# Kernel tuning notes

Measured on AMD Instinct MI355X. Metric: run time of the kernel, lower is better.

Reference implementation:

```python
import jax, jax.numpy as jnp
import numpy as np

COEF_MEMORY = 0.2

def setup_inputs() -> dict:
    key = jax.random.key(0)
    k1, k2, k3, k4 = jax.random.split(key, 4)
    B, T, HW, C, Cv, M = 2, 8, 4096, 64, 3, 1024
    k = jax.random.normal(k1, (B, T, HW, C), dtype=jnp.float32)
    v = jax.random.normal(k2, (B, T, HW, Cv), dtype=jnp.float32)
    m_k = jax.random.normal(k3, (B, T - 1, M, C), dtype=jnp.float32)
    m_v = jax.random.normal(k4, (B, T - 1, M, Cv), dtype=jnp.float32)
    return {"k": k, "v": v, "m_k": m_k, "m_v": m_v}

def reference(k, v, m_k, m_v):
    # k: [B,T,HW,C] frame keys; v: [B,T,HW,Cv] frame values (quarter-res images)
    # m_k: [B,T-1,M,C] memory keys at step i; m_v: [B,T-1,M,Cv] memory values
    c = COEF_MEMORY
    k_i = k[:, :-1]  # ref keys  [B,T-1,HW,C]
    k_j = k[:, 1:]   # tar keys  [B,T-1,HW,C]
    v_i = v[:, :-1]  # ref vals  [B,T-1,HW,Cv]
    # frame-to-frame affinity: softmax over ref positions (last axis)
    sim_k = jax.nn.softmax(jnp.einsum('btqc,btkc->btqk', k_j, k_i), axis=-1)
    # memory-to-frame affinity: softmax over memory slots
    sim_m = jax.nn.softmax(jnp.einsum('btqc,btmc->btqm', k_j, m_k), axis=-1)
    rec_k = jnp.einsum('btqk,btkd->btqd', sim_k, v_i)   # [B,T-1,HW,Cv]
    rec_m = jnp.einsum('btqm,btmd->btqd', sim_m, m_v)   # [B,T-1,HW,Cv]
    return (1.0 - c) * rec_k + c * rec_m
```

## Files before the change

### kernel.cpp

```cpp
#include <hip/hip_runtime.h>

typedef __attribute__((ext_vector_type(2))) __fp16 h2;
typedef __attribute__((ext_vector_type(4))) __fp16 h4;
typedef __attribute__((ext_vector_type(8))) __fp16 h8;
typedef __attribute__((ext_vector_type(4))) float f32x4;

#define LOG2E 1.44269504088896340736f

#define WS_K    0ull
#define WS_MK   7340032ull
#define WS_VT   9175040ull
#define WS_MVT  9633792ull
#define WS_NEED 9748480ull

__device__ __forceinline__ h2 pkrtz(float a, float b) {
    return __builtin_bit_cast(h2, __builtin_amdgcn_cvt_pkrtz(a, b));
}

__device__ __forceinline__ void gll16(const void* g, void* l) {
    __builtin_amdgcn_global_load_lds(
        (const __attribute__((address_space(1))) unsigned int*)g,
        (__attribute__((address_space(3))) unsigned int*)l, 16, 0, 0);
}

__global__ __launch_bounds__(256) void kast_pre_kernel(
    const float* __restrict__ K, const float* __restrict__ V,
    const float* __restrict__ MK, const float* __restrict__ MV,
    char* __restrict__ ws)
{
    const int id = blockIdx.x * 256 + threadIdx.x;
    if (id < 573440) {
        const bool ismk = id >= 458752;
        const int lid = ismk ? id - 458752 : id;
        const int c = lid & 7;
        const int r = (lid >> 3) & 63;
        int kt, s;
        if (ismk) { kt = (lid >> 9) & 15; s = lid >> 13; }
        else      { kt = (lid >> 9) & 63; s = lid >> 15; }
        const int b = s / 7, t = s - b * 7;
        const float* src = ismk
            ? MK + (((size_t)(b * 7 + t) * 1024 + kt * 64 + r) * 64 + c * 8)
            : K  + (((size_t)(b * 8 + t) * 4096 + kt * 64 + r) * 64 + c * 8);
        const f32x4 xa = *(const f32x4*)src;
        const f32x4 xb = *(const f32x4*)(src + 4);
        const h2 q0 = pkrtz(xa[0], xa[1]), q1 = pkrtz(xa[2], xa[3]);
        const h2 q2 = pkrtz(xb[0], xb[1]), q3 = pkrtz(xb[2], xb[3]);
        const h8 out = {q0[0], q0[1], q1[0], q1[1], q2[0], q2[1], q3[0], q3[1]};
        __fp16* dst = (__fp16*)(ws + (ismk ? WS_MK : WS_K))
                    + (size_t)(ismk ? (s * 16 + kt) : (s * 64 + kt)) * 4096
                    + r * 64 + ((c ^ (r & 7)) * 8);
        *(h8*)dst = out;
    } else {
        const int vid = id - 573440;
        const bool ismv = vid >= 57344;
        const int lid = ismv ? vid - 57344 : vid;
        const int c = lid & 15;
        const int d = (lid >> 4) & 3;
        int kt, s;
        if (ismv) { kt = (lid >> 6) & 15; s = lid >> 10; }
        else      { kt = (lid >> 6) & 63; s = lid >> 12; }
        const int b = s / 7, t = s - b * 7;
        const float* src = ismv
            ? MV + (((size_t)(b * 7 + t) * 1024 + kt * 64 + c * 4) * 3)
            : V  + (((size_t)(b * 8 + t) * 4096 + kt * 64 + c * 4) * 3);
        float f0, f1, f2, f3;
        if (d == 3) { f0 = f1 = f2 = f3 = 1.0f; }
        else { f0 = src[d]; f1 = src[3 + d]; f2 = src[6 + d]; f3 = src[9 + d]; }
        const h2 pa = pkrtz(f0, f1), pb = pkrtz(f2, f3);
        const h4 out4 = {pa[0], pa[1], pb[0], pb[1]};
        __fp16* dst = (__fp16*)(ws + (ismv ? WS_MVT : WS_VT))
                    + (size_t)(ismv ? (s * 16 + kt) : (s * 64 + kt)) * 256
                    + d * 64 + (4 * ((c >> 2) ^ d) + (c & 3)) * 4;
        *(h4*)dst = out4;
    }
}

__global__ __launch_bounds__(512) void kast_attn_kernel(
    const float* __restrict__ K,
    const char* __restrict__ ws,
    float* __restrict__ OUT)
{
    __shared__ alignas(16) __fp16 sK2[2][2][64][64];
    __shared__ alignas(16) __fp16 sVT2[2][2][4][64];
    __shared__ float mrg[8][16][10];

    const int id = blockIdx.x;
    const int sw = (id & 7) * 112 + (id >> 3);
    const int bt = sw >> 6;
    const int qblk = sw & 63;
    const int b = bt / 7, t = bt - b * 7;

    const int tid = threadIdx.x;
    const int lane = tid & 63;
    const int w = tid >> 6;
    const int h = w >> 2;
    const int wl = w & 3;
    const int col = lane & 15;
    const int g = lane >> 4;
    const int cs = col & 7;
    const int d3 = col & 3;

    const float* qp = K + (((size_t)b * 8 + (t + 1)) * 4096 + (size_t)(qblk * 64 + wl * 16 + col)) * 64;
    h8 aq[2];
#pragma unroll
    for (int ch = 0; ch < 2; ++ch) {
        const int cc = ch * 32 + g * 8;
        const f32x4 xa = *(const f32x4*)&qp[cc];
        const f32x4 xb = *(const f32x4*)&qp[cc + 4];
        const h2 p0 = pkrtz(xa[0] * LOG2E, xa[1] * LOG2E);
        const h2 p1 = pkrtz(xa[2] * LOG2E, xa[3] * LOG2E);
        const h2 p2 = pkrtz(xb[0] * LOG2E, xb[1] * LOG2E);
        const h2 p3 = pkrtz(xb[2] * LOG2E, xb[3] * LOG2E);
        aq[ch] = (h8){p0[0], p0[1], p1[0], p1[1], p2[0], p2[1], p3[0], p3[1]};
    }

    auto stage = [&](const char* kb, const char* vb, int tkt, int buf) {
        const char* ksrc = kb + (size_t)tkt * 8192 + wl * 2048 + lane * 16;
        char* kdst = ((char*)&sK2[h][buf][0][0]) + wl * 2048 + lane * 16;
        gll16(ksrc, kdst);
        gll16(ksrc + 1024, kdst + 1024);
        if (wl == 0 && lane < 32)
            ((f32x4*)&sVT2[h][buf][0][0])[lane] =
                ((const f32x4*)(vb + (size_t)tkt * 512))[lane];
    };

#pragma unroll
    for (int phase = 0; phase < 2; ++phase) {
        const char* kbase; const char* vbase; int ntile;
        if (phase == 0) {
            ntile = 32;
            kbase = ws + WS_K  + ((size_t)bt * 64 + h * 32) * 8192;
            vbase = ws + WS_VT + ((size_t)bt * 64 + h * 32) * 512;
        } else {
            ntile = 8;
            kbase = ws + WS_MK  + ((size_t)bt * 16 + h * 8) * 8192;
            vbase = ws + WS_MVT + ((size_t)bt * 16 + h * 8) * 512;
        }

        stage(kbase, vbase, 0, 0);
        __syncthreads();

        float mrun = -1e30f;
        f32x4 O = (f32x4){0.f, 0.f, 0.f, 0.f};

        for (int kt = 0; kt < ntile; ++kt) {
            const int cur = kt & 1;
            const int nb = cur ^ 1;

            if (kt + 1 < ntile) stage(kbase, vbase, kt + 1, nb);

            f32x4 acc[4];
#pragma unroll
            for (int nt = 0; nt < 4; ++nt) acc[nt] = (f32x4){0.f, 0.f, 0.f, 0.f};
            __builtin_amdgcn_s_setprio(1);
#pragma unroll
            for (int ch = 0; ch < 2; ++ch) {
                h8 bh[4];
#pragma unroll
                for (int nt = 0; nt < 4; ++nt)
                    bh[nt] = *(const h8*)&sK2[h][cur][nt * 16 + col][((ch * 4 + g) ^ cs) * 8];
#pragma unroll
                for (int nt = 0; nt < 4; ++nt)
                    acc[nt] = __builtin_amdgcn_mfma_f32_16x16x32_f16(bh[nt], aq[ch], acc[nt], 0, 0, 0);
            }
            __builtin_amdgcn_s_setprio(0);

            {
                float tm = acc[0][0];
#pragma unroll
                for (int nt = 0; nt < 4; ++nt)
#pragma unroll
                    for (int j = 0; j < 4; ++j) tm = fmaxf(tm, acc[nt][j]);
                tm = fmaxf(tm, __shfl_xor(tm, 16));
                tm = fmaxf(tm, __shfl_xor(tm, 32));
                if (!__all(tm <= mrun)) {
                    const float mnew = fmaxf(mrun, tm);
                    const float sc = __builtin_amdgcn_exp2f(mrun - mnew);
                    O *= sc;
                    mrun = mnew;
                }
            }

            const char* vtb = (const char*)&sVT2[h][cur][0][0] + d3 * 128;
#pragma unroll
            for (int nt = 0; nt < 4; ++nt) {
                const float p0 = __builtin_amdgcn_exp2f(acc[nt][0] - mrun);
                const float p1 = __builtin_amdgcn_exp2f(acc[nt][1] - mrun);
                const float p2 = __builtin_amdgcn_exp2f(acc[nt][2] - mrun);
                const float p3 = __builtin_amdgcn_exp2f(acc[nt][3] - mrun);
                const h2 pa = pkrtz(p0, p1), pb = pkrtz(p2, p3);
                const h4 pf = (h4){pa[0], pa[1], pb[0], pb[1]};
                const h4 vf = *(const h4*)(vtb + (4 * (nt ^ d3) + g) * 8);
                O = __builtin_amdgcn_mfma_f32_16x16x16f16(vf, pf, O, 0, 0, 0);
            }

            __syncthreads();
        }

        if (g == 0) {
            float* m5 = &mrg[w][col][phase * 5];
            m5[0] = mrun; m5[1] = O[0]; m5[2] = O[1]; m5[3] = O[2]; m5[4] = O[3];
        }
    }

    __syncthreads();
    if (w < 4 && g == 0) {
        const float* A = &mrg[w][col][0];
        const float* B = &mrg[w + 4][col][0];
        float o0 = 0.f, o1 = 0.f, o2 = 0.f;
#pragma unroll
        for (int p = 0; p < 2; ++p) {
            const float wgt = p ? 0.2f : 0.8f;
            const float ma = A[p * 5], mb = B[p * 5];
            const float m = fmaxf(ma, mb);
            const float ea = __builtin_amdgcn_exp2f(ma - m);
            const float eb = __builtin_amdgcn_exp2f(mb - m);
            const float l = A[p * 5 + 4] * ea + B[p * 5 + 4] * eb;
            const float inv = wgt / l;
            o0 += (A[p * 5 + 1] * ea + B[p * 5 + 1] * eb) * inv;
            o1 += (A[p * 5 + 2] * ea + B[p * 5 + 2] * eb) * inv;
            o2 += (A[p * 5 + 3] * ea + B[p * 5 + 3] * eb) * inv;
        }
        const int q = qblk * 64 + w * 16 + col;
        float* op = OUT + (((size_t)b * 7 + t) * 4096 + (size_t)q) * 3;
        op[0] = o0; op[1] = o1; op[2] = o2;
    }
}

__global__ __launch_bounds__(256) void kast_attn_fb(
    const float* __restrict__ K, const float* __restrict__ V,
    const float* __restrict__ MK, const float* __restrict__ MV,
    float* __restrict__ OUT)
{
    __shared__ alignas(16) __fp16 sK[2][64][64];
    __shared__ alignas(16) __fp16 sVT[2][4][68];

    const int id = blockIdx.x;
    const int sw = (id & 7) * 112 + (id >> 3);
    const int bt = sw >> 6;
    const int qblk = sw & 63;
    const int b = bt / 7, t = bt % 7;

    const int tid = threadIdx.x;
    const int lane = tid & 63;
    const int w = tid >> 6;
    const int col = lane & 15;
    const int g = lane >> 4;

    const int r = tid >> 2;
    const int c0 = (tid & 3) * 16;
    const int rs = (r & 7) << 3;
    const unsigned vr = (unsigned)tid / 3u;
    const unsigned vd = (unsigned)tid - vr * 3u;

    if (tid < 128) sVT[tid >> 6][3][tid & 63] = (__fp16)1.0f;

    const float* Qbase = K + (((size_t)b * 8 + (t + 1)) * 4096) * 64;
    h8 aq[2];
    {
        const int qrow = qblk * 64 + w * 16 + col;
        const float* qp = Qbase + (size_t)qrow * 64;
#pragma unroll
        for (int ch = 0; ch < 2; ++ch) {
            const int cc = ch * 32 + g * 8;
            const f32x4 xa = *(const f32x4*)&qp[cc];
            const f32x4 xb = *(const f32x4*)&qp[cc + 4];
            const h2 p0 = pkrtz(xa[0] * LOG2E, xa[1] * LOG2E);
            const h2 p1 = pkrtz(xa[2] * LOG2E, xa[3] * LOG2E);
            const h2 p2 = pkrtz(xb[0] * LOG2E, xb[1] * LOG2E);
            const h2 p3 = pkrtz(xb[2] * LOG2E, xb[3] * LOG2E);
            aq[ch] = (h8){p0[0], p0[1], p1[0], p1[1], p2[0], p2[1], p3[0], p3[1]};
        }
    }

    float outc0 = 0.f, outc1 = 0.f, outc2 = 0.f;

    for (int phase = 0; phase < 2; ++phase) {
        const float* kp; const float* vp; int ntile; float wgt;
        if (phase == 0) {
            kp = K + (((size_t)b * 8 + t) * 4096) * 64;
            vp = V + (((size_t)b * 8 + t) * 4096) * 3;
            ntile = 64; wgt = 0.8f;
        } else {
            kp = MK + (((size_t)b * 7 + t) * 1024) * 64;
            vp = MV + (((size_t)b * 7 + t) * 1024) * 3;
            ntile = 16; wgt = 0.2f;
        }
        {
            const float* src = kp + ((size_t)r) * 64 + c0;
            const f32x4* s4 = (const f32x4*)src;
            const f32x4 ra = s4[0], rb = s4[1], rc = s4[2], rd = s4[3];
            const h2 q0 = pkrtz(ra[0], ra[1]), q1 = pkrtz(ra[2], ra[3]);
            const h2 q2 = pkrtz(rb[0], rb[1]), q3 = pkrtz(rb[2], rb[3]);
            const h2 q4 = pkrtz(rc[0], rc[1]), q5 = pkrtz(rc[2], rc[3]);
            const h2 q6 = pkrtz(rd[0], rd[1]), q7 = pkrtz(rd[2], rd[3]);
            *(h8*)&sK[0][r][c0 ^ rs] = (h8){q0[0], q0[1], q1[0], q1[1], q2[0], q2[1], q3[0], q3[1]};
            *(h8*)&sK[0][r][(c0 + 8) ^ rs] = (h8){q4[0], q4[1], q5[0], q5[1], q6[0], q6[1], q7[0], q7[1]};
            if (tid < 192) sVT[0][vd][vr] = (__fp16)vp[tid];
        }
        __syncthreads();

        float mrun = -1e30f;
        f32x4 O = (f32x4){0.f, 0.f, 0.f, 0.f};

        for (int kt = 0; kt < ntile; ++kt) {
            const int cur = kt & 1;
            const bool have = (kt + 1) < ntile;
            f32x4 ra, rb, rc, rd; float rv = 0.f;
            if (have) {
                const float* src = kp + ((size_t)(kt + 1) * 64 + r) * 64 + c0;
                const f32x4* s4 = (const f32x4*)src;
                ra = s4[0]; rb = s4[1]; rc = s4[2]; rd = s4[3];
                if (tid < 192) rv = vp[(size_t)(kt + 1) * 192 + tid];
            }
            f32x4 acc[4];
#pragma unroll
            for (int nt = 0; nt < 4; ++nt) acc[nt] = (f32x4){0.f, 0.f, 0.f, 0.f};
#pragma unroll
            for (int ch = 0; ch < 2; ++ch) {
                h8 bh[4];
#pragma unroll
                for (int nt = 0; nt < 4; ++nt) {
                    const int rr = nt * 16 + col;
                    const int cc = (ch * 32 + g * 8) ^ ((rr & 7) << 3);
                    bh[nt] = *(const h8*)&sK[cur][rr][cc];
                }
#pragma unroll
                for (int nt = 0; nt < 4; ++nt)
                    acc[nt] = __builtin_amdgcn_mfma_f32_16x16x32_f16(bh[nt], aq[ch], acc[nt], 0, 0, 0);
            }
            {
                float tm = acc[0][0];
#pragma unroll
                for (int nt = 0; nt < 4; ++nt)
#pragma unroll
                    for (int j = 0; j < 4; ++j) tm = fmaxf(tm, acc[nt][j]);
                tm = fmaxf(tm, __shfl_xor(tm, 16));
                tm = fmaxf(tm, __shfl_xor(tm, 32));
                if (!__all(tm <= mrun)) {
                    const float mnew = fmaxf(mrun, tm);
                    const float sc = __builtin_amdgcn_exp2f(mrun - mnew);
                    O *= sc;
                    mrun = mnew;
                }
            }
#pragma unroll
            for (int nt = 0; nt < 4; ++nt) {
                const float p0 = __builtin_amdgcn_exp2f(acc[nt][0] - mrun);
                const float p1 = __builtin_amdgcn_exp2f(acc[nt][1] - mrun);
                const float p2 = __builtin_amdgcn_exp2f(acc[nt][2] - mrun);
                const float p3 = __builtin_amdgcn_exp2f(acc[nt][3] - mrun);
                const h2 pa = pkrtz(p0, p1), pb = pkrtz(p2, p3);
                const h4 pf = (h4){pa[0], pa[1], pb[0], pb[1]};
                const h4 vf = *(const h4*)&sVT[cur][col & 3][nt * 16 + 4 * g];
                O = __builtin_amdgcn_mfma_f32_16x16x16f16(vf, pf, O, 0, 0, 0);
            }
            if (have) {
                const int nb = cur ^ 1;
                const h2 q0 = pkrtz(ra[0], ra[1]), q1 = pkrtz(ra[2], ra[3]);
                const h2 q2 = pkrtz(rb[0], rb[1]), q3 = pkrtz(rb[2], rb[3]);
                const h2 q4 = pkrtz(rc[0], rc[1]), q5 = pkrtz(rc[2], rc[3]);
                const h2 q6 = pkrtz(rd[0], rd[1]), q7 = pkrtz(rd[2], rd[3]);
                *(h8*)&sK[nb][r][c0 ^ rs] = (h8){q0[0], q0[1], q1[0], q1[1], q2[0], q2[1], q3[0], q3[1]};
                *(h8*)&sK[nb][r][(c0 + 8) ^ rs] = (h8){q4[0], q4[1], q5[0], q5[1], q6[0], q6[1], q7[0], q7[1]};
                if (tid < 192) sVT[nb][vd][vr] = (__fp16)rv;
            }
            __syncthreads();
        }
        const float inv = wgt / O[3];
        outc0 += O[0] * inv;
        outc1 += O[1] * inv;
        outc2 += O[2] * inv;
    }

    if (g == 0) {
        const int q = qblk * 64 + w * 16 + col;
        float* op = OUT + (((size_t)b * 7 + t) * 4096 + (size_t)q) * 3;
        op[0] = outc0; op[1] = outc1; op[2] = outc2;
    }
}

extern "C" void kernel_launch(void* const* d_in, const int* in_sizes, int n_in,
                              void* d_out, int out_size, void* d_ws, size_t ws_size,
                              hipStream_t stream) {
    const float* K  = (const float*)d_in[0];
    const float* V  = (const float*)d_in[1];
    const float* MK = (const float*)d_in[2];
    const float* MV = (const float*)d_in[3];
    float* OUT = (float*)d_out;
    if (ws_size >= WS_NEED) {
        hipLaunchKernelGGL(kast_pre_kernel, dim3(2520), dim3(256), 0, stream,
                           K, V, MK, MV, (char*)d_ws);
        hipLaunchKernelGGL(kast_attn_kernel, dim3(896), dim3(512), 0, stream,
                           K, (const char*)d_ws, OUT);
    } else {
        hipLaunchKernelGGL(kast_attn_fb, dim3(896), dim3(256), 0, stream,
                           K, V, MK, MV, OUT);
    }
}
```

Before: 96.87 us.

## Retile waves to 2x2 query-key MFMA tiles with four-way softmax merge

Measured after the change: 118.1 us. +21.9%, slower.

```diff
diff --git a/kernel.cpp b/kernel.cpp
--- a/kernel.cpp
+++ b/kernel.cpp
@@ -82,7 +82,7 @@
 {
     __shared__ alignas(16) __fp16 sK2[2][2][64][64];
     __shared__ alignas(16) __fp16 sVT2[2][2][4][64];
-    __shared__ float mrg[8][16][10];
+    __shared__ float mrg[8][32][5];
 
     const int id = blockIdx.x;
     const int sw = (id & 7) * 112 + (id >> 3);
@@ -95,23 +95,29 @@
     const int w = tid >> 6;
     const int h = w >> 2;
     const int wl = w & 3;
+    const int qsub = wl >> 1;
+    const int ntp = wl & 1;
     const int col = lane & 15;
     const int g = lane >> 4;
     const int cs = col & 7;
     const int d3 = col & 3;
 
-    const float* qp = K + (((size_t)b * 8 + (t + 1)) * 4096 + (size_t)(qblk * 64 + wl * 16 + col)) * 64;
-    h8 aq[2];
-#pragma unroll
-    for (int ch = 0; ch < 2; ++ch) {
-        const int cc = ch * 32 + g * 8;
-        const f32x4 xa = *(const f32x4*)&qp[cc];
-        const f32x4 xb = *(const f32x4*)&qp[cc + 4];
-        const h2 p0 = pkrtz(xa[0] * LOG2E, xa[1] * LOG2E);
-        const h2 p1 = pkrtz(xa[2] * LOG2E, xa[3] * LOG2E);
-        const h2 p2 = pkrtz(xb[0] * LOG2E, xb[1] * LOG2E);
-        const h2 p3 = pkrtz(xb[2] * LOG2E, xb[3] * LOG2E);
-        aq[ch] = (h8){p0[0], p0[1], p1[0], p1[1], p2[0], p2[1], p3[0], p3[1]};
+    h8 aq[2][2];
+#pragma unroll
+    for (int mt = 0; mt < 2; ++mt) {
+        const float* qp = K + (((size_t)b * 8 + (t + 1)) * 4096
+                         + (size_t)(qblk * 64 + qsub * 32 + mt * 16 + col)) * 64;
+#pragma unroll
+        for (int ch = 0; ch < 2; ++ch) {
+            const int cc = ch * 32 + g * 8;
+            const f32x4 xa = *(const f32x4*)&qp[cc];
+            const f32x4 xb = *(const f32x4*)&qp[cc + 4];
+            const h2 p0 = pkrtz(xa[0] * LOG2E, xa[1] * LOG2E);
+            const h2 p1 = pkrtz(xa[2] * LOG2E, xa[3] * LOG2E);
+            const h2 p2 = pkrtz(xb[0] * LOG2E, xb[1] * LOG2E);
+            const h2 p3 = pkrtz(xb[2] * LOG2E, xb[3] * LOG2E);
+            aq[mt][ch] = (h8){p0[0], p0[1], p1[0], p1[1], p2[0], p2[1], p3[0], p3[1]};
+        }
     }
 
     auto stage = [&](const char* kb, const char* vb, int tkt, int buf) {
@@ -124,15 +130,17 @@
                 ((const f32x4*)(vb + (size_t)tkt * 512))[lane];
     };
 
+    float oa0 = 0.f, oa1 = 0.f, oa2 = 0.f;
+
 #pragma unroll
     for (int phase = 0; phase < 2; ++phase) {
-        const char* kbase; const char* vbase; int ntile;
+        const char* kbase; const char* vbase; int ntile; float wgt;
         if (phase == 0) {
-            ntile = 32;
+            ntile = 32; wgt = 0.8f;
             kbase = ws + WS_K  + ((size_t)bt * 64 + h * 32) * 8192;
             vbase = ws + WS_VT + ((size_t)bt * 64 + h * 32) * 512;
         } else {
-            ntile = 8;
+            ntile = 8; wgt = 0.2f;
             kbase = ws + WS_MK  + ((size_t)bt * 16 + h * 8) * 8192;
             vbase = ws + WS_MVT + ((size_t)bt * 16 + h * 8) * 512;
         }
@@ -140,90 +148,104 @@
         stage(kbase, vbase, 0, 0);
         __syncthreads();
 
-        float mrun = -1e30f;
-        f32x4 O = (f32x4){0.f, 0.f, 0.f, 0.f};
+        float mrun[2] = {-1e30f, -1e30f};
+        f32x4 O[2] = {(f32x4){0.f,0.f,0.f,0.f}, (f32x4){0.f,0.f,0.f,0.f}};
 
         for (int kt = 0; kt < ntile; ++kt) {
             const int cur = kt & 1;
-            const int nb = cur ^ 1;
-
-            if (kt + 1 < ntile) stage(kbase, vbase, kt + 1, nb);
-
-            f32x4 acc[4];
-#pragma unroll
-            for (int nt = 0; nt < 4; ++nt) acc[nt] = (f32x4){0.f, 0.f, 0.f, 0.f};
+
+            if (kt + 1 < ntile) stage(kbase, vbase, kt + 1, cur ^ 1);
+
+            f32x4 acc[2][2];
+#pragma unroll
+            for (int mt = 0; mt < 2; ++mt)
+#pragma unroll
+                for (int nt = 0; nt < 2; ++nt) acc[mt][nt] = (f32x4){0.f,0.f,0.f,0.f};
             __builtin_amdgcn_s_setprio(1);
 #pragma unroll
             for (int ch = 0; ch < 2; ++ch) {
-                h8 bh[4];
-#pragma unroll
-                for (int nt = 0; nt < 4; ++nt)
-                    bh[nt] = *(const h8*)&sK2[h][cur][nt * 16 + col][((ch * 4 + g) ^ cs) * 8];
-#pragma unroll
-                for (int nt = 0; nt < 4; ++nt)
-                    acc[nt] = __builtin_amdgcn_mfma_f32_16x16x32_f16(bh[nt], aq[ch], acc[nt], 0, 0, 0);
+                h8 bh[2];
+#pragma unroll
+                for (int nt = 0; nt < 2; ++nt) {
+                    const int nt2 = ntp * 2 + nt;
+                    bh[nt] = *(const h8*)&sK2[h][cur][nt2 * 16 + col][((ch * 4 + g) ^ cs) * 8];
+                }
+#pragma unroll
+                for (int mt = 0; mt < 2; ++mt)
+#pragma unroll
+                    for (int nt = 0; nt < 2; ++nt)
+                        acc[mt][nt] = __builtin_amdgcn_mfma_f32_16x16x32_f16(bh[nt], aq[mt][ch], acc[mt][nt], 0, 0, 0);
             }
             __builtin_amdgcn_s_setprio(0);
 
-            {
-                float tm = acc[0][0];
-#pragma unroll
-                for (int nt = 0; nt < 4; ++nt)
-#pragma unroll
-                    for (int j = 0; j < 4; ++j) tm = fmaxf(tm, acc[nt][j]);
+            const char* vtb = (const char*)&sVT2[h][cur][0][0] + d3 * 128;
+#pragma unroll
+            for (int mt = 0; mt < 2; ++mt) {
+                float tm = acc[mt][0][0];
+#pragma unroll
+                for (int nt = 0; nt < 2; ++nt)
+#pragma unroll
+                    for (int j = 0; j < 4; ++j) tm = fmaxf(tm, acc[mt][nt][j]);
                 tm = fmaxf(tm, __shfl_xor(tm, 16));
                 tm = fmaxf(tm, __shfl_xor(tm, 32));
-                if (!__all(tm <= mrun)) {
-                    const float mnew = fmaxf(mrun, tm);
-                    const float sc = __builtin_amdgcn_exp2f(mrun - mnew);
-                    O *= sc;
-                    mrun = mnew;
+                if (!__all(tm <= mrun[mt])) {
+                    const float mnew = fmaxf(mrun[mt], tm);
+                    const float sc = __builtin_amdgcn_exp2f(mrun[mt] - mnew);
+                    O[mt] *= sc;
+                    mrun[mt] = mnew;
                 }
-            }
-
-            const char* vtb = (const char*)&sVT2[h][cur][0][0] + d3 * 128;
-#pragma unroll
-            for (int nt = 0; nt < 4; ++nt) {
-                const float p0 = __builtin_amdgcn_exp2f(acc[nt][0] - mrun);
-                const float p1 = __builtin_amdgcn_exp2f(acc[nt][1] - mrun);
-                const float p2 = __builtin_amdgcn_exp2f(acc[nt][2] - mrun);
-                const float p3 = __builtin_amdgcn_exp2f(acc[nt][3] - mrun);
-                const h2 pa = pkrtz(p0, p1), pb = pkrtz(p2, p3);
-                const h4 pf = (h4){pa[0], pa[1], pb[0], pb[1]};
-                const h4 vf = *(const h4*)(vtb + (4 * (nt ^ d3) + g) * 8);
-                O = __builtin_amdgcn_mfma_f32_16x16x16f16(vf, pf, O, 0, 0, 0);
+#pragma unroll
+                for (int nt = 0; nt < 2; ++nt) {
+                    const int nt2 = ntp * 2 + nt;
+                    const float p0 = __builtin_amdgcn_exp2f(acc[mt][nt][0] - mrun[mt]);
+                    const float p1 = __builtin_amdgcn_exp2f(acc[mt][nt][1] - mrun[mt]);
+                    const float p2 = __builtin_amdgcn_exp2f(acc[mt][nt][2] - mrun[mt]);
+                    const float p3 = __builtin_amdgcn_exp2f(acc[mt][nt][3] - mrun[mt]);
+                    const h2 pa = pkrtz(p0, p1), pb = pkrtz(p2, p3);
+                    const h4 pf = (h4){pa[0], pa[1], pb[0], pb[1]};
+                    const h4 vf = *(const h4*)(vtb + (4 * (nt2 ^ d3) + g) * 8);
+                    O[mt] = __builtin_amdgcn_mfma_f32_16x16x16f16(vf, pf, O[mt], 0, 0, 0);
+                }
             }
 
             __syncthreads();
         }
 
         if (g == 0) {
-            float* m5 = &mrg[w][col][phase * 5];
-            m5[0] = mrun; m5[1] = O[0]; m5[2] = O[1]; m5[3] = O[2]; m5[4] = O[3];
-        }
-    }
-
-    __syncthreads();
-    if (w < 4 && g == 0) {
-        const float* A = &mrg[w][col][0];
-        const float* B = &mrg[w + 4][col][0];
-        float o0 = 0.f, o1 = 0.f, o2 = 0.f;
-#pragma unroll
-        for (int p = 0; p < 2; ++p) {
-            const float wgt = p ? 0.2f : 0.8f;
-            const float ma = A[p * 5], mb = B[p * 5];
-            const float m = fmaxf(ma, mb);
-            const float ea = __builtin_amdgcn_exp2f(ma - m);
-            const float eb = __builtin_amdgcn_exp2f(mb - m);
-            const float l = A[p * 5 + 4] * ea + B[p * 5 + 4] * eb;
+#pragma unroll
+            for (int mt = 0; mt < 2; ++mt) {
+                float* m5 = &mrg[w][mt * 16 + col][0];
+                m5[0] = mrun[mt];
+                m5[1] = O[mt][0]; m5[2] = O[mt][1]; m5[3] = O[mt][2]; m5[4] = O[mt][3];
+            }
+        }
+        __syncthreads();
+        if (tid < 64) {
+            const int qh = tid >> 5, ql = tid & 31;
+            float m = -1e30f;
+#pragma unroll
+            for (int c = 0; c < 4; ++c) {
+                const int w4 = (c >> 1) * 4 + qh * 2 + (c & 1);
+                m = fmaxf(m, mrg[w4][ql][0]);
+            }
+            float l = 0.f, r0 = 0.f, r1 = 0.f, r2 = 0.f;
+#pragma unroll
+            for (int c = 0; c < 4; ++c) {
+                const int w4 = (c >> 1) * 4 + qh * 2 + (c & 1);
+                const float* m5 = &mrg[w4][ql][0];
+                const float e = __builtin_amdgcn_exp2f(m5[0] - m);
+                r0 += m5[1] * e; r1 += m5[2] * e; r2 += m5[3] * e;
+                l  += m5[4] * e;
+            }
             const float inv = wgt / l;
-            o0 += (A[p * 5 + 1] * ea + B[p * 5 + 1] * eb) * inv;
-            o1 += (A[p * 5 + 2] * ea + B[p * 5 + 2] * eb) * inv;
-            o2 += (A[p * 5 + 3] * ea + B[p * 5 + 3] * eb) * inv;
-        }
-        const int q = qblk * 64 + w * 16 + col;
+            oa0 += r0 * inv; oa1 += r1 * inv; oa2 += r2 * inv;
+        }
+    }
+
+    if (tid < 64) {
+        const int q = qblk * 64 + tid;
         float* op = OUT + (((size_t)b * 7 + t) * 4096 + (size_t)q) * 3;
-        op[0] = o0; op[1] = o1; op[2] = o2;
+        op[0] = oa0; op[1] = oa1; op[2] = oa2;
     }
 }
 
```
